# Optimization experiments

Measured on AMD Instinct MI355X. Metric: run time of the kernel, lower is better.

## Reference

```python
import jax, jax.numpy as jnp
import numpy as np

COMMITMENT_COST = 0.25
EPS = 1e-10


def setup_inputs() -> dict:
    key = jax.random.key(0)
    k1, k2 = jax.random.split(key)
    z_e = jax.random.normal(k1, (64, 4096, 64), dtype=jnp.float32)
    codebook = jax.random.normal(k2, (1024, 64), dtype=jnp.float32)
    return {"z_e": z_e, "codebook": codebook}


def reference(z_e, codebook):
    K, d = codebook.shape
    z_flat = z_e.reshape(-1, d)                      # [N, d]
    N = z_flat.shape[0]
    # squared L2 distances: ||z||^2 + ||e||^2 - 2 z.e  -> [N, K]
    distances = (jnp.sum(z_flat ** 2, axis=1, keepdims=True)
                 + jnp.sum(codebook ** 2, axis=1)
                 - 2.0 * jnp.matmul(z_flat, codebook.T))
    idx = jnp.argmin(distances, axis=1)              # [N]
    # direct gather (equivalent to one-hot @ codebook)
    z_q_flat = codebook[idx]                         # [N, d]
    z_q = z_q_flat.reshape(z_e.shape)
    e_latent_loss = jnp.mean((jax.lax.stop_gradient(z_q) - z_e) ** 2)
    q_latent_loss = jnp.mean((z_q - jax.lax.stop_gradient(z_e)) ** 2)
    loss = q_latent_loss + COMMITMENT_COST * e_latent_loss
    # avg one-hot probs via scatter-add (counts / N)
    counts = jnp.zeros((K,), dtype=jnp.float32).at[idx].add(1.0)
    avg_probs = counts / N
    perplexity = jnp.exp(-jnp.sum(avg_probs * jnp.log(avg_probs + EPS)))
    # straight-through estimator
    z_q_st = z_e + jax.lax.stop_gradient(z_q - z_e)
    return (z_q_st, loss, perplexity)
```

## Files before the change

kernel.cpp:

```cpp
#include <hip/hip_runtime.h>
#include <math.h>

#define NROWS   (64 * 4096)
#define D       64
#define K       1024
#define NELEM   ((size_t)NROWS * (size_t)D)

#define CHUNK_CODES 128
#define ROWB        144
#define CBH_BYTES   (CHUNK_CODES * ROWB)
#define REC_BYTES   (CBH_BYTES * 2 + 512)
#define NCHUNK      (K / CHUNK_CODES)
#define WS_CHUNK_OFF 16384
#define WS_MAIN_NEED (WS_CHUNK_OFF + NCHUNK * REC_BYTES)
#define BLK_ROWS    128
#define NBLOCKS     (NROWS / BLK_ROWS)

#define GAP_THRESH 8.0e-3f

typedef float  f32x4  __attribute__((ext_vector_type(4)));
typedef short  s16x8  __attribute__((ext_vector_type(8)));


static __device__ inline unsigned bf16_rne(unsigned u) {
  return (u + 0x7FFFu + ((u >> 16) & 1u)) >> 16;
}

__global__ __launch_bounds__(256) void vq_prep(const float* __restrict__ cb,
                                               char* __restrict__ ws) {
  int k = blockIdx.x * 256 + threadIdx.x;
  if (k >= K) return;
  int chunk = k >> 7, cc = k & 127;
  char* rec = ws + WS_CHUNK_OFF + chunk * REC_BYTES;
  unsigned short* hrow = (unsigned short*)(rec + cc * ROWB);
  unsigned short* lrow = (unsigned short*)(rec + CBH_BYTES + cc * ROWB);
  const float* src = cb + (k << 6);
  float nrm = 0.f;
  for (int j = 0; j < 64; j += 2) {
    float x0 = src[j], x1 = src[j + 1];
    nrm = fmaf(x0, x0, fmaf(x1, x1, nrm));
    unsigned h0 = bf16_rne(__float_as_uint(x0));
    unsigned h1 = bf16_rne(__float_as_uint(x1));
    float hf0 = __uint_as_float(h0 << 16), hf1 = __uint_as_float(h1 << 16);
    unsigned l0 = bf16_rne(__float_as_uint(x0 - hf0));
    unsigned l1 = bf16_rne(__float_as_uint(x1 - hf1));
    *(unsigned*)(hrow + j) = h0 | (h1 << 16);
    *(unsigned*)(lrow + j) = l0 | (l1 << 16);
  }
  *(float*)(rec + 2 * CBH_BYTES + cc * 4) = nrm;
}

__global__ __launch_bounds__(256, 4) void vq_mfma(const float* __restrict__ z,
                                                  const float* __restrict__ cb,
                                                  const char* __restrict__ ws,
                                                  float* __restrict__ zq,
                                                  unsigned int* __restrict__ counts,
                                                  float* __restrict__ block_loss) {
  __shared__ __align__(16) char sblob[REC_BYTES];
  __shared__ int   sk[BLK_ROWS];
  __shared__ float red[256];

  const int t    = threadIdx.x;
  const int w    = t >> 6;
  const int lane = t & 63;
  const int g    = lane >> 4;
  const int ln16 = lane & 15;

  const int rowbase = blockIdx.x * BLK_ROWS + w * 32;
  s16x8 zh[2][2], zl[2][2];
#pragma unroll
  for (int rt = 0; rt < 2; ++rt) {
    int row = rowbase + rt * 16 + ln16;
    const float4* zr = (const float4*)(z + row * 64);
#pragma unroll
    for (int ks = 0; ks < 2; ++ks) {
      float4 a = zr[ks * 8 + g * 2];
      float4 b = zr[ks * 8 + g * 2 + 1];
      float xs[8] = {a.x, a.y, a.z, a.w, b.x, b.y, b.z, b.w};
      s16x8 hh, ll;
#pragma unroll
      for (int j = 0; j < 8; ++j) {
        unsigned hb = bf16_rne(__float_as_uint(xs[j]));
        float hf = __uint_as_float(hb << 16);
        unsigned lb = bf16_rne(__float_as_uint(xs[j] - hf));
        hh[j] = (short)hb; ll[j] = (short)lb;
      }
      zh[rt][ks] = hh; zl[rt][ks] = ll;
    }
  }

  float m1v0 = 3.4e38f, m2v0 = 3.4e38f, m3v0 = 3.4e38f;
  float m1v1 = 3.4e38f, m2v1 = 3.4e38f, m3v1 = 3.4e38f;
  int   m1i0 = 0, m2i0 = 0, m1i1 = 0, m2i1 = 0;

  const int aoff = ln16 * ROWB + g * 16;

  for (int c = 0; c < NCHUNK; ++c) {
    __syncthreads();
    {
      const float4* src = (const float4*)(ws + WS_CHUNK_OFF + c * REC_BYTES);
      float4* dst = (float4*)sblob;
#pragma unroll
      for (int i = 0; i < 10; ++i) {
        int idx = t + 256 * i;
        if (idx < REC_BYTES / 16) dst[idx] = src[idx];
      }
    }
    __syncthreads();

#pragma unroll
    for (int tl = 0; tl < CHUNK_CODES / 16; ++tl) {
      const char* ab = sblob + tl * 16 * ROWB + aoff;
      s16x8 eh0 = *(const s16x8*)(ab);
      s16x8 eh1 = *(const s16x8*)(ab + 64);
      s16x8 el0 = *(const s16x8*)(ab + CBH_BYTES);
      s16x8 el1 = *(const s16x8*)(ab + CBH_BYTES + 64);
      f32x4 nrm = *(const f32x4*)(sblob + 2 * CBH_BYTES + tl * 64 + g * 16);

      f32x4 acc0 = {0.f, 0.f, 0.f, 0.f}, acc1 = {0.f, 0.f, 0.f, 0.f};
      acc0 = __builtin_amdgcn_mfma_f32_16x16x32_bf16(eh0, zh[0][0], acc0, 0, 0, 0);
      acc1 = __builtin_amdgcn_mfma_f32_16x16x32_bf16(eh0, zh[1][0], acc1, 0, 0, 0);
      acc0 = __builtin_amdgcn_mfma_f32_16x16x32_bf16(eh1, zh[0][1], acc0, 0, 0, 0);
      acc1 = __builtin_amdgcn_mfma_f32_16x16x32_bf16(eh1, zh[1][1], acc1, 0, 0, 0);
      acc0 = __builtin_amdgcn_mfma_f32_16x16x32_bf16(el0, zh[0][0], acc0, 0, 0, 0);
      acc1 = __builtin_amdgcn_mfma_f32_16x16x32_bf16(el0, zh[1][0], acc1, 0, 0, 0);
      acc0 = __builtin_amdgcn_mfma_f32_16x16x32_bf16(el1, zh[0][1], acc0, 0, 0, 0);
      acc1 = __builtin_amdgcn_mfma_f32_16x16x32_bf16(el1, zh[1][1], acc1, 0, 0, 0);
      acc0 = __builtin_amdgcn_mfma_f32_16x16x32_bf16(eh0, zl[0][0], acc0, 0, 0, 0);
      acc1 = __builtin_amdgcn_mfma_f32_16x16x32_bf16(eh0, zl[1][0], acc1, 0, 0, 0);
      acc0 = __builtin_amdgcn_mfma_f32_16x16x32_bf16(eh1, zl[0][1], acc0, 0, 0, 0);
      acc1 = __builtin_amdgcn_mfma_f32_16x16x32_bf16(eh1, zl[1][1], acc1, 0, 0, 0);

      const int kbase = c * CHUNK_CODES + tl * 16 + g * 4;
#define UPD(RT, R) {                                                        \
        float m = fmaf(-2.f, acc##RT[R], nrm[R]);                           \
        int   kk = kbase + R;                                               \
        bool lt1 = m < m1v##RT;                                             \
        bool lt2 = m < m2v##RT;                                             \
        float o1v = m1v##RT; int o1i = m1i##RT; float o2v = m2v##RT;        \
        m3v##RT = fminf(m3v##RT, fmaxf(o2v, m));                            \
        m2v##RT = lt1 ? o1v : (lt2 ? m : o2v);                              \
        m2i##RT = lt1 ? o1i : (lt2 ? kk : m2i##RT);                         \
        m1v##RT = lt1 ? m : o1v;                                            \
        m1i##RT = lt1 ? kk : o1i;                                           \
      }
      UPD(0, 0) UPD(0, 1) UPD(0, 2) UPD(0, 3)
      UPD(1, 0) UPD(1, 1) UPD(1, 2) UPD(1, 3)
#undef UPD
    }
  }

  const float4* cb4 = (const float4*)cb;
  const float4* z4g = (const float4*)z;
#pragma unroll
  for (int rt = 0; rt < 2; ++rt) {
    float m1 = rt ? m1v1 : m1v0;  int i1 = rt ? m1i1 : m1i0;
    float m2 = rt ? m2v1 : m2v0;  int i2 = rt ? m2i1 : m2i0;
    float m3 = rt ? m3v1 : m3v0;
#pragma unroll
    for (int dx = 16; dx <= 32; dx <<= 1) {
      float o1 = __shfl_xor(m1, dx); int oi1 = __shfl_xor(i1, dx);
      float o2 = __shfl_xor(m2, dx); int oi2 = __shfl_xor(i2, dx);
      float o3 = __shfl_xor(m3, dx);
      float nm3 = fminf(fminf(m3, o3), fminf(fmaxf(m2, o1), fmaxf(o2, m1)));
      bool take1 = (o1 < m1) || (o1 == m1 && oi1 < i1);
      float hi1v = take1 ? m1 : o1; int hi1i = take1 ? i1 : oi1;
      float nm1  = take1 ? o1 : m1; int ni1  = take1 ? oi1 : i1;
      bool h2 = (m2 < o2) || (m2 == o2 && i2 < oi2);
      float c2v = h2 ? m2 : o2; int c2i = h2 ? i2 : oi2;
      bool hb2 = (hi1v < c2v) || (hi1v == c2v && hi1i < c2i);
      float nm2 = hb2 ? hi1v : c2v; int ni2 = hb2 ? hi1i : c2i;
      m1 = nm1; i1 = ni1; m2 = nm2; i2 = ni2; m3 = nm3;
    }
    bool needFull = (m3 - m1) < GAP_THRESH;
    bool needPair = !needFull && ((m2 - m1) < GAP_THRESH);
    int  kstar = i1;

    if (g == 0) {
      int row = rowbase + rt * 16 + ln16;
      if (needPair) {
        float d1 = 0.f, d2 = 0.f;
        const float4* zr = z4g + row * 16;
        const float4* c1 = cb4 + i1 * 16;
        const float4* c2 = cb4 + i2 * 16;
#pragma unroll
        for (int j = 0; j < 16; ++j) {
          float4 zv = zr[j], a = c1[j], b = c2[j];
          float e;
          e = zv.x - a.x; d1 = fmaf(e, e, d1);
          e = zv.y - a.y; d1 = fmaf(e, e, d1);
          e = zv.z - a.z; d1 = fmaf(e, e, d1);
          e = zv.w - a.w; d1 = fmaf(e, e, d1);
          e = zv.x - b.x; d2 = fmaf(e, e, d2);
          e = zv.y - b.y; d2 = fmaf(e, e, d2);
          e = zv.z - b.z; d2 = fmaf(e, e, d2);
          e = zv.w - b.w; d2 = fmaf(e, e, d2);
        }
        if (d2 < d1 || (d2 == d1 && i2 < i1)) kstar = i2;
      }
      if (!needFull) {
        int lrow = w * 32 + rt * 16 + ln16;
        sk[lrow] = kstar;
        atomicAdd(&counts[kstar], 1u);
      }
    }

    unsigned long long fullmask = __ballot(needFull && g == 0);
    while (fullmask) {
      int src = __ffsll(fullmask) - 1;
      fullmask &= fullmask - 1;
      int lrow = w * 32 + rt * 16 + src;
      int row  = blockIdx.x * BLK_ROWS + lrow;
      const float4* zr = z4g + row * 16;
      float bv = 3.4e38f; int bi = 0;
      for (int c16 = 0; c16 < 16; ++c16) {
        int code = c16 * 64 + lane;
        const float4* cr = cb4 + code * 16;
        float d = 0.f;
#pragma unroll
        for (int j = 0; j < 16; ++j) {
          float4 zv = zr[j], cv = cr[j];
          float e;
          e = zv.x - cv.x; d = fmaf(e, e, d);
          e = zv.y - cv.y; d = fmaf(e, e, d);
          e = zv.z - cv.z; d = fmaf(e, e, d);
          e = zv.w - cv.w; d = fmaf(e, e, d);
        }
        if (d < bv) { bv = d; bi = code; }
      }
#pragma unroll
      for (int dx = 1; dx < 64; dx <<= 1) {
        float ov = __shfl_xor(bv, dx); int oi = __shfl_xor(bi, dx);
        if (ov < bv || (ov == bv && oi < bi)) { bv = ov; bi = oi; }
      }
      if (lane == 0) { sk[lrow] = bi; atomicAdd(&counts[bi], 1u); }
    }
  }

  __syncthreads();

  float lpart = 0.f;
  const int base4 = blockIdx.x * (BLK_ROWS * 16);
  float4* out4 = (float4*)zq;
#pragma unroll
  for (int i = 0; i < 8; ++i) {
    int idx = t + 256 * i;
    int row = idx >> 4, c4 = idx & 15;
    int kk = sk[row];
    float4 cv = cb4[kk * 16 + c4];
    float4 zv = z4g[base4 + idx];
    float e;
    e = zv.x - cv.x; lpart = fmaf(e, e, lpart);
    e = zv.y - cv.y; lpart = fmaf(e, e, lpart);
    e = zv.z - cv.z; lpart = fmaf(e, e, lpart);
    e = zv.w - cv.w; lpart = fmaf(e, e, lpart);
    out4[base4 + idx] = cv;
  }
  red[t] = lpart;
  __syncthreads();
#pragma unroll
  for (int s = 128; s > 0; s >>= 1) {
    if (t < s) red[t] += red[t + s];
    __syncthreads();
  }
  if (t == 0) block_loss[blockIdx.x] = red[0];
}

__global__ __launch_bounds__(1024) void vq_finalize(const unsigned int* __restrict__ counts,
                                                    const float* __restrict__ block_loss,
                                                    float* __restrict__ out, int nb) {
  __shared__ float sh[1024];
  __shared__ float sl[1024];
  const int t = threadIdx.x;
  float c = (float)counts[t];
  float p = c * (1.0f / (float)NROWS);
  sh[t] = p * logf(p + 1e-10f);
  float bl = (t < nb) ? block_loss[t] : 0.f;
  if (t + 1024 < nb) bl += block_loss[t + 1024];
  sl[t] = bl;
  __syncthreads();
#pragma unroll
  for (int s = 512; s > 0; s >>= 1) {
    if (t < s) { sh[t] += sh[t + s]; sl[t] += sl[t + s]; }
    __syncthreads();
  }
  if (t == 0) {
    out[NELEM]     = 1.25f * sl[0] / (float)NELEM;
    out[NELEM + 1] = expf(-sh[0]);
  }
}

#define DOT4(acc, a, e) \
  acc = fmaf((a).x, (e).x, fmaf((a).y, (e).y, fmaf((a).z, (e).z, fmaf((a).w, (e).w, (acc)))))
#define SQD4(acc, a, e) { \
  float _dx = (e).x - (a).x, _dy = (e).y - (a).y, _dz = (e).z - (a).z, _dw = (e).w - (a).w; \
  acc = fmaf(_dx, _dx, fmaf(_dy, _dy, fmaf(_dz, _dz, fmaf(_dw, _dw, (acc))))); }

__global__ __launch_bounds__(256) void vq_norms_fb(const float* __restrict__ cb,
                                                   float* __restrict__ norms) {
  int k = blockIdx.x * blockDim.x + threadIdx.x;
  if (k >= K) return;
  const float4* e4 = (const float4*)(cb + (k << 6));
  float a0 = 0.f, a1 = 0.f, a2 = 0.f, a3 = 0.f;
#pragma unroll
  for (int j = 0; j < 16; j += 4) {
    float4 e;
    e = e4[j + 0]; DOT4(a0, e, e);
    e = e4[j + 1]; DOT4(a1, e, e);
    e = e4[j + 2]; DOT4(a2, e, e);
    e = e4[j + 3]; DOT4(a3, e, e);
  }
  norms[k] = (a0 + a1) + (a2 + a3);
}

__global__ __launch_bounds__(256) void vq_main_fb(const float* __restrict__ z,
                                                  const float* __restrict__ cb,
                                                  const float* __restrict__ norms,
                                                  float* __restrict__ zq,
                                                  unsigned int* __restrict__ counts,
                                                  float* __restrict__ block_loss) {
  const int tid = threadIdx.x;
  const int row = blockIdx.x * 256 + tid;
  const float4* zr4 = (const float4*)(z + (size_t)row * D);
  float4 zr[16];
#pragma unroll
  for (int j = 0; j < 16; ++j) zr[j] = zr4[j];
  float best = 3.4e38f;
  int   bidx = 0;
  for (int k = 0; k < K; k += 2) {
    const float4* e0 = (const float4*)(cb + (k << 6));
    const float4* e1 = e0 + 16;
    float a0 = 0.f, a1 = 0.f, a2 = 0.f, a3 = 0.f;
    float b0 = 0.f, b1 = 0.f, b2 = 0.f, b3 = 0.f;
#pragma unroll
    for (int j = 0; j < 16; j += 4) {
      float4 tt;
      tt = e0[j + 0]; DOT4(a0, zr[j + 0], tt);
      tt = e1[j + 0]; DOT4(b0, zr[j + 0], tt);
      tt = e0[j + 1]; DOT4(a1, zr[j + 1], tt);
      tt = e1[j + 1]; DOT4(b1, zr[j + 1], tt);
      tt = e0[j + 2]; DOT4(a2, zr[j + 2], tt);
      tt = e1[j + 2]; DOT4(b2, zr[j + 2], tt);
      tt = e0[j + 3]; DOT4(a3, zr[j + 3], tt);
      tt = e1[j + 3]; DOT4(b3, zr[j + 3], tt);
    }
    float d0 = (a0 + a1) + (a2 + a3);
    float d1 = (b0 + b1) + (b2 + b3);
    float m0 = fmaf(-2.f, d0, norms[k]);
    float m1 = fmaf(-2.f, d1, norms[k + 1]);
    if (m0 < best) { best = m0; bidx = k; }
    if (m1 < best) { best = m1; bidx = k + 1; }
  }
  const float4* eb4 = (const float4*)(cb + ((size_t)bidx << 6));
  float4* o4 = (float4*)(zq + (size_t)row * D);
  float l0 = 0.f, l1 = 0.f, l2 = 0.f, l3 = 0.f;
#pragma unroll
  for (int j = 0; j < 16; j += 4) {
    float4 e;
    e = eb4[j + 0]; o4[j + 0] = e; SQD4(l0, zr[j + 0], e);
    e = eb4[j + 1]; o4[j + 1] = e; SQD4(l1, zr[j + 1], e);
    e = eb4[j + 2]; o4[j + 2] = e; SQD4(l2, zr[j + 2], e);
    e = eb4[j + 3]; o4[j + 3] = e; SQD4(l3, zr[j + 3], e);
  }
  float row_loss = (l0 + l1) + (l2 + l3);
  atomicAdd(&counts[bidx], 1u);
  __shared__ float redf[256];
  redf[tid] = row_loss;
  __syncthreads();
#pragma unroll
  for (int s = 128; s > 0; s >>= 1) {
    if (tid < s) redf[tid] += redf[tid + s];
    __syncthreads();
  }
  if (tid == 0) block_loss[blockIdx.x] = redf[0];
}

extern "C" void kernel_launch(void* const* d_in, const int* in_sizes, int n_in,
                              void* d_out, int out_size, void* d_ws, size_t ws_size,
                              hipStream_t stream) {
  const float* z  = (const float*)d_in[0];
  const float* cb = (const float*)d_in[1];
  float* out = (float*)d_out;

  unsigned int* counts     = (unsigned int*)d_ws;
  float*        block_loss = (float*)((char*)d_ws + 4096);

  hipMemsetAsync(d_ws, 0, 4096, stream);

  if (ws_size >= WS_MAIN_NEED) {
    vq_prep<<<dim3(4), dim3(256), 0, stream>>>(cb, (char*)d_ws);
    vq_mfma<<<dim3(NBLOCKS), dim3(256), 0, stream>>>(z, cb, (const char*)d_ws,
                                                     out, counts, block_loss);
    vq_finalize<<<dim3(1), dim3(1024), 0, stream>>>(counts, block_loss, out, NBLOCKS);
  } else {
    float* norms = (float*)((char*)d_ws + 12288);
    vq_norms_fb<<<dim3(4), dim3(256), 0, stream>>>(cb, norms);
    vq_main_fb<<<dim3(NROWS / 256), dim3(256), 0, stream>>>(z, cb, norms,
                                                            out, counts, block_loss);
    vq_finalize<<<dim3(1), dim3(1024), 0, stream>>>(counts, block_loss, out, 1024);
  }
}
```

Before: 199.6 us.

## Use single bf16 distance pass with packed value-index keys and wider gap

Drops the hi/lo bf16 split so each tile needs 4 MFMAs instead of 12, and relies on a wider gap threshold (0.8) to route ambiguous rows to exact fp32 pair or full rechecks. The top-3 tracking now packs each distance and its code index into one unsigned key. The norms get a positive bias so the float bits order correctly as unsigneds. Shared memory is halved and reused for the epilogue, and occupancy is raised to 8 blocks. The risk is that many more rows fall into the exact fallback paths, and that truncating the low 10 mantissa bits loses ordering precision.

```diff
diff --git a/kernel.cpp b/kernel.cpp
--- a/kernel.cpp
+++ b/kernel.cpp
@@ -8,15 +8,16 @@
 
 #define CHUNK_CODES 128
 #define ROWB        144
-#define CBH_BYTES   (CHUNK_CODES * ROWB)
-#define REC_BYTES   (CBH_BYTES * 2 + 512)
+#define REC_USED    (CHUNK_CODES * ROWB + 512)
+#define REC_BYTES   20480
 #define NCHUNK      (K / CHUNK_CODES)
 #define WS_CHUNK_OFF 16384
 #define WS_MAIN_NEED (WS_CHUNK_OFF + NCHUNK * REC_BYTES)
 #define BLK_ROWS    128
 #define NBLOCKS     (NROWS / BLK_ROWS)
 
-#define GAP_THRESH 8.0e-3f
+#define MBIAS  256.0f
+#define GAP_Q  0.8f
 
 typedef float  f32x4  __attribute__((ext_vector_type(4)));
 typedef short  s16x8  __attribute__((ext_vector_type(8)));
@@ -25,6 +26,8 @@
 static __device__ inline unsigned bf16_rne(unsigned u) {
   return (u + 0x7FFFu + ((u >> 16) & 1u)) >> 16;
 }
+static __device__ inline unsigned umin_(unsigned a, unsigned b) { return a < b ? a : b; }
+static __device__ inline unsigned umax_(unsigned a, unsigned b) { return a > b ? a : b; }
 
 __global__ __launch_bounds__(256) void vq_prep(const float* __restrict__ cb,
                                                char* __restrict__ ws) {
@@ -33,7 +36,6 @@
   int chunk = k >> 7, cc = k & 127;
   char* rec = ws + WS_CHUNK_OFF + chunk * REC_BYTES;
   unsigned short* hrow = (unsigned short*)(rec + cc * ROWB);
-  unsigned short* lrow = (unsigned short*)(rec + CBH_BYTES + cc * ROWB);
   const float* src = cb + (k << 6);
   float nrm = 0.f;
   for (int j = 0; j < 64; j += 2) {
@@ -41,24 +43,18 @@
     nrm = fmaf(x0, x0, fmaf(x1, x1, nrm));
     unsigned h0 = bf16_rne(__float_as_uint(x0));
     unsigned h1 = bf16_rne(__float_as_uint(x1));
-    float hf0 = __uint_as_float(h0 << 16), hf1 = __uint_as_float(h1 << 16);
-    unsigned l0 = bf16_rne(__float_as_uint(x0 - hf0));
-    unsigned l1 = bf16_rne(__float_as_uint(x1 - hf1));
     *(unsigned*)(hrow + j) = h0 | (h1 << 16);
-    *(unsigned*)(lrow + j) = l0 | (l1 << 16);
-  }
-  *(float*)(rec + 2 * CBH_BYTES + cc * 4) = nrm;
-}
-
-__global__ __launch_bounds__(256, 4) void vq_mfma(const float* __restrict__ z,
+  }
+  *(float*)(rec + CHUNK_CODES * ROWB + cc * 4) = nrm + MBIAS;
+}
+
+__global__ __launch_bounds__(256, 8) void vq_mfma(const float* __restrict__ z,
                                                   const float* __restrict__ cb,
                                                   const char* __restrict__ ws,
                                                   float* __restrict__ zq,
                                                   unsigned int* __restrict__ counts,
                                                   float* __restrict__ block_loss) {
   __shared__ __align__(16) char sblob[REC_BYTES];
-  __shared__ int   sk[BLK_ROWS];
-  __shared__ float red[256];
 
   const int t    = threadIdx.x;
   const int w    = t >> 6;
@@ -67,31 +63,25 @@
   const int ln16 = lane & 15;
 
   const int rowbase = blockIdx.x * BLK_ROWS + w * 32;
-  s16x8 zh[2][2], zl[2][2];
+  s16x8 zh[2][2];
 #pragma unroll
   for (int rt = 0; rt < 2; ++rt) {
     int row = rowbase + rt * 16 + ln16;
-    const float4* zr = (const float4*)(z + row * 64);
+    const float4* zr = (const float4*)(z + (size_t)row * 64);
 #pragma unroll
     for (int ks = 0; ks < 2; ++ks) {
       float4 a = zr[ks * 8 + g * 2];
       float4 b = zr[ks * 8 + g * 2 + 1];
       float xs[8] = {a.x, a.y, a.z, a.w, b.x, b.y, b.z, b.w};
-      s16x8 hh, ll;
-#pragma unroll
-      for (int j = 0; j < 8; ++j) {
-        unsigned hb = bf16_rne(__float_as_uint(xs[j]));
-        float hf = __uint_as_float(hb << 16);
-        unsigned lb = bf16_rne(__float_as_uint(xs[j] - hf));
-        hh[j] = (short)hb; ll[j] = (short)lb;
-      }
-      zh[rt][ks] = hh; zl[rt][ks] = ll;
-    }
-  }
-
-  float m1v0 = 3.4e38f, m2v0 = 3.4e38f, m3v0 = 3.4e38f;
-  float m1v1 = 3.4e38f, m2v1 = 3.4e38f, m3v1 = 3.4e38f;
-  int   m1i0 = 0, m2i0 = 0, m1i1 = 0, m2i1 = 0;
+      s16x8 hh;
+#pragma unroll
+      for (int j = 0; j < 8; ++j) hh[j] = (short)bf16_rne(__float_as_uint(xs[j]));
+      zh[rt][ks] = hh;
+    }
+  }
+
+  unsigned q1a = ~0u, q2a = ~0u, q3a = ~0u;
+  unsigned q1b = ~0u, q2b = ~0u, q3b = ~0u;
 
   const int aoff = ln16 * ROWB + g * 16;
 
@@ -101,9 +91,9 @@
       const float4* src = (const float4*)(ws + WS_CHUNK_OFF + c * REC_BYTES);
       float4* dst = (float4*)sblob;
 #pragma unroll
-      for (int i = 0; i < 10; ++i) {
+      for (int i = 0; i < 5; ++i) {
         int idx = t + 256 * i;
-        if (idx < REC_BYTES / 16) dst[idx] = src[idx];
+        if (idx < REC_USED / 16) dst[idx] = src[idx];
       }
     }
     __syncthreads();
@@ -113,74 +103,65 @@
       const char* ab = sblob + tl * 16 * ROWB + aoff;
       s16x8 eh0 = *(const s16x8*)(ab);
       s16x8 eh1 = *(const s16x8*)(ab + 64);
-      s16x8 el0 = *(const s16x8*)(ab + CBH_BYTES);
-      s16x8 el1 = *(const s16x8*)(ab + CBH_BYTES + 64);
-      f32x4 nrm = *(const f32x4*)(sblob + 2 * CBH_BYTES + tl * 64 + g * 16);
+      f32x4 nr  = *(const f32x4*)(sblob + CHUNK_CODES * ROWB + tl * 64 + g * 16);
 
       f32x4 acc0 = {0.f, 0.f, 0.f, 0.f}, acc1 = {0.f, 0.f, 0.f, 0.f};
       acc0 = __builtin_amdgcn_mfma_f32_16x16x32_bf16(eh0, zh[0][0], acc0, 0, 0, 0);
       acc1 = __builtin_amdgcn_mfma_f32_16x16x32_bf16(eh0, zh[1][0], acc1, 0, 0, 0);
       acc0 = __builtin_amdgcn_mfma_f32_16x16x32_bf16(eh1, zh[0][1], acc0, 0, 0, 0);
       acc1 = __builtin_amdgcn_mfma_f32_16x16x32_bf16(eh1, zh[1][1], acc1, 0, 0, 0);
-      acc0 = __builtin_amdgcn_mfma_f32_16x16x32_bf16(el0, zh[0][0], acc0, 0, 0, 0);
-      acc1 = __builtin_amdgcn_mfma_f32_16x16x32_bf16(el0, zh[1][0], acc1, 0, 0, 0);
-      acc0 = __builtin_amdgcn_mfma_f32_16x16x32_bf16(el1, zh[0][1], acc0, 0, 0, 0);
-      acc1 = __builtin_amdgcn_mfma_f32_16x16x32_bf16(el1, zh[1][1], acc1, 0, 0, 0);
-      acc0 = __builtin_amdgcn_mfma_f32_16x16x32_bf16(eh0, zl[0][0], acc0, 0, 0, 0);
-      acc1 = __builtin_amdgcn_mfma_f32_16x16x32_bf16(eh0, zl[1][0], acc1, 0, 0, 0);
-      acc0 = __builtin_amdgcn_mfma_f32_16x16x32_bf16(eh1, zl[0][1], acc0, 0, 0, 0);
-      acc1 = __builtin_amdgcn_mfma_f32_16x16x32_bf16(eh1, zl[1][1], acc1, 0, 0, 0);
-
-      const int kbase = c * CHUNK_CODES + tl * 16 + g * 4;
-#define UPD(RT, R) {                                                        \
-        float m = fmaf(-2.f, acc##RT[R], nrm[R]);                           \
-        int   kk = kbase + R;                                               \
-        bool lt1 = m < m1v##RT;                                             \
-        bool lt2 = m < m2v##RT;                                             \
-        float o1v = m1v##RT; int o1i = m1i##RT; float o2v = m2v##RT;        \
-        m3v##RT = fminf(m3v##RT, fmaxf(o2v, m));                            \
-        m2v##RT = lt1 ? o1v : (lt2 ? m : o2v);                              \
-        m2i##RT = lt1 ? o1i : (lt2 ? kk : m2i##RT);                         \
-        m1v##RT = lt1 ? m : o1v;                                            \
-        m1i##RT = lt1 ? kk : o1i;                                           \
-      }
-      UPD(0, 0) UPD(0, 1) UPD(0, 2) UPD(0, 3)
-      UPD(1, 0) UPD(1, 1) UPD(1, 2) UPD(1, 3)
-#undef UPD
-    }
-  }
+
+      const unsigned kb = (unsigned)((c << 7) + (tl << 4) + (g << 2));
+#define UPDP(S, RT, R) {                                                    \
+        float m = fmaf(-2.f, acc##RT[R], nr[R]);                            \
+        unsigned key = (__float_as_uint(m) & 0xFFFFFC00u) | (kb + R);       \
+        unsigned t1 = umax_(q1##S, key); q1##S = umin_(q1##S, key);         \
+        unsigned t2 = umax_(q2##S, t1);  q2##S = umin_(q2##S, t1);         \
+        q3##S = umin_(q3##S, t2); }
+      UPDP(a, 0, 0) UPDP(a, 0, 1) UPDP(a, 0, 2) UPDP(a, 0, 3)
+      UPDP(b, 1, 0) UPDP(b, 1, 1) UPDP(b, 1, 2) UPDP(b, 1, 3)
+#undef UPDP
+    }
+  }
+
+  __syncthreads();
+  int*   sk  = (int*)sblob;
+  float* red = (float*)(sblob + 512);
 
   const float4* cb4 = (const float4*)cb;
   const float4* z4g = (const float4*)z;
+
 #pragma unroll
   for (int rt = 0; rt < 2; ++rt) {
-    float m1 = rt ? m1v1 : m1v0;  int i1 = rt ? m1i1 : m1i0;
-    float m2 = rt ? m2v1 : m2v0;  int i2 = rt ? m2i1 : m2i0;
-    float m3 = rt ? m3v1 : m3v0;
+    unsigned a1 = rt ? q1b : q1a;
+    unsigned a2 = rt ? q2b : q2a;
+    unsigned a3 = rt ? q3b : q3a;
 #pragma unroll
     for (int dx = 16; dx <= 32; dx <<= 1) {
-      float o1 = __shfl_xor(m1, dx); int oi1 = __shfl_xor(i1, dx);
-      float o2 = __shfl_xor(m2, dx); int oi2 = __shfl_xor(i2, dx);
-      float o3 = __shfl_xor(m3, dx);
-      float nm3 = fminf(fminf(m3, o3), fminf(fmaxf(m2, o1), fmaxf(o2, m1)));
-      bool take1 = (o1 < m1) || (o1 == m1 && oi1 < i1);
-      float hi1v = take1 ? m1 : o1; int hi1i = take1 ? i1 : oi1;
-      float nm1  = take1 ? o1 : m1; int ni1  = take1 ? oi1 : i1;
-      bool h2 = (m2 < o2) || (m2 == o2 && i2 < oi2);
-      float c2v = h2 ? m2 : o2; int c2i = h2 ? i2 : oi2;
-      bool hb2 = (hi1v < c2v) || (hi1v == c2v && hi1i < c2i);
-      float nm2 = hb2 ? hi1v : c2v; int ni2 = hb2 ? hi1i : c2i;
-      m1 = nm1; i1 = ni1; m2 = nm2; i2 = ni2; m3 = nm3;
-    }
-    bool needFull = (m3 - m1) < GAP_THRESH;
-    bool needPair = !needFull && ((m2 - m1) < GAP_THRESH);
+      unsigned b1 = (unsigned)__shfl_xor((int)a1, dx);
+      unsigned b2 = (unsigned)__shfl_xor((int)a2, dx);
+      unsigned b3 = (unsigned)__shfl_xor((int)a3, dx);
+      unsigned x  = umax_(a1, b1);
+      a1 = umin_(a1, b1);
+      unsigned y  = umin_(a2, b2);
+      unsigned zz = umax_(a2, b2);
+      unsigned w3 = umin_(a3, b3);
+      a2 = umin_(x, y);
+      a3 = umin_(umax_(x, y), umin_(zz, w3));
+    }
+    int   i1 = (int)(a1 & 1023u), i2 = (int)(a2 & 1023u);
+    float f1 = __uint_as_float(a1 & 0xFFFFFC00u);
+    float f2 = __uint_as_float(a2 & 0xFFFFFC00u);
+    float f3 = __uint_as_float(a3 & 0xFFFFFC00u);
+    bool needFull = (f3 - f1) < GAP_Q;
+    bool needPair = !needFull && ((f2 - f1) < GAP_Q);
     int  kstar = i1;
 
     if (g == 0) {
       int row = rowbase + rt * 16 + ln16;
       if (needPair) {
         float d1 = 0.f, d2 = 0.f;
-        const float4* zr = z4g + row * 16;
+        const float4* zr = z4g + (size_t)row * 16;
         const float4* c1 = cb4 + i1 * 16;
         const float4* c2 = cb4 + i2 * 16;
 #pragma unroll
@@ -199,8 +180,7 @@
         if (d2 < d1 || (d2 == d1 && i2 < i1)) kstar = i2;
       }
       if (!needFull) {
-        int lrow = w * 32 + rt * 16 + ln16;
-        sk[lrow] = kstar;
+        sk[w * 32 + rt * 16 + ln16] = kstar;
         atomicAdd(&counts[kstar], 1u);
       }
     }
@@ -211,7 +191,7 @@
       fullmask &= fullmask - 1;
       int lrow = w * 32 + rt * 16 + src;
       int row  = blockIdx.x * BLK_ROWS + lrow;
-      const float4* zr = z4g + row * 16;
+      const float4* zr = z4g + (size_t)row * 16;
       float bv = 3.4e38f; int bi = 0;
       for (int c16 = 0; c16 < 16; ++c16) {
         int code = c16 * 64 + lane;
```

Measured after the change: 497.2 us. 149% more time.
